# Kernel tuning notes

Hardware: AMD Instinct MI355X
Metric: run time of the kernel (lower is better)

The kernel has to match this reference:

```python
import jax, jax.numpy as jnp
import numpy as np

N = 40000   # nodes
E = 480000  # edges
F = 128     # input features
H = 128     # hidden
C = 10      # classes
G = 128     # graphs in batch
L = 3       # conv layers
EPS = 1e-5


def _bn(x, g, b):
    # BatchNorm1d, training-mode batch statistics (biased variance, as torch)
    m = x.mean(0)
    v = x.var(0)
    return (x - m) / jnp.sqrt(v + EPS) * g + b


def _gcn_prop(x, row, col, w, n):
    # PyG-style GCN propagation: add self loops (weight 1), sym-normalize, scatter-add.
    loop = jnp.arange(n)
    r = jnp.concatenate([row, loop])
    c = jnp.concatenate([col, loop])
    ww = jnp.concatenate([w, jnp.ones((n,), x.dtype)])
    deg = jax.ops.segment_sum(ww, r, num_segments=n)  # deg >= 1 thanks to self loops
    dinv = jnp.power(deg, -0.5)
    norm = dinv[r] * ww * dinv[c]                      # [E+N]
    return jax.ops.segment_sum(norm[:, None] * x[r], c, num_segments=n)


def setup_inputs() -> dict:
    key = jax.random.key(0)
    ks = jax.random.split(key, 12)
    nrm = lambda k, s: jax.random.normal(k, s, jnp.float32) * 0.02
    return {
        'x': jax.random.normal(ks[0], (N, F), jnp.float32),
        'edge_index': jax.random.randint(ks[1], (2, E), 0, N, jnp.int32),
        'batch': jnp.sort(jax.random.randint(ks[2], (N,), 0, G, jnp.int32)),
        'bn_feat_g': jnp.ones((F,), jnp.float32), 'bn_feat_b': jnp.full((F,), 1e-4, jnp.float32),
        'W_feat': nrm(ks[3], (F, H)),
        'bns_g': jnp.ones((L, H), jnp.float32), 'bns_b': jnp.full((L, H), 1e-4, jnp.float32),
        'conv_W': nrm(ks[4], (L, H, H)), 'conv_b': jnp.zeros((L, H), jnp.float32),
        'W_eatt': nrm(ks[5], (2 * H, 2)), 'b_eatt': jnp.zeros((2,), jnp.float32),
        'W_natt': nrm(ks[6], (H, 2)), 'b_natt': jnp.zeros((2,), jnp.float32),
        'bnc_g': jnp.ones((H,), jnp.float32), 'bnc_b': jnp.full((H,), 1e-4, jnp.float32),
        'bno_g': jnp.ones((H,), jnp.float32), 'bno_b': jnp.full((H,), 1e-4, jnp.float32),
        'Wc': nrm(ks[7], (H, H)), 'bc': jnp.zeros((H,), jnp.float32),
        'Wo': nrm(ks[8], (H, H)), 'bo': jnp.zeros((H,), jnp.float32),
        'ro_bn1_g': jnp.ones((3, H), jnp.float32), 'ro_bn1_b': jnp.full((3, H), 1e-4, jnp.float32),
        'ro_W1': nrm(ks[9], (3, H, H)), 'ro_b1': jnp.zeros((3, H), jnp.float32),
        'ro_bn2_g': jnp.ones((3, H), jnp.float32), 'ro_bn2_b': jnp.full((3, H), 1e-4, jnp.float32),
        'ro_W2': nrm(ks[10], (3, H, C)), 'ro_b2': jnp.zeros((3, C), jnp.float32),
    }


def reference(x, edge_index, batch,
              bn_feat_g, bn_feat_b, W_feat, bns_g, bns_b, conv_W, conv_b,
              W_eatt, b_eatt, W_natt, b_natt, bnc_g, bnc_b, bno_g, bno_b,
              Wc, bc, Wo, bo,
              ro_bn1_g, ro_bn1_b, ro_W1, ro_b1, ro_bn2_g, ro_bn2_b, ro_W2, ro_b2):
    row, col = edge_index[0], edge_index[1]
    # feature BN + gfn conv (linear only, no propagation, no bias) + ReLU
    h = jax.nn.relu(_bn(x, bn_feat_g, bn_feat_b) @ W_feat)
    ones_w = jnp.ones((E,), h.dtype)
    for i in range(L):
        z = _bn(h, bns_g[i], bns_b[i]) @ conv_W[i]
        h = jax.nn.relu(_gcn_prop(z, row, col, ones_w, N) + conv_b[i])
    # edge / node attention
    edge_rep = jnp.concatenate([h[row], h[col]], axis=-1)          # [E, 2H]
    e_att = jax.nn.softmax(edge_rep @ W_eatt + b_eatt, axis=-1)    # [E, 2]
    n_att = jax.nn.softmax(h @ W_natt + b_natt, axis=-1)           # [N, 2]
    xc = n_att[:, 0:1] * h
    xo = n_att[:, 1:2] * h
    xc = jax.nn.relu(_gcn_prop(_bn(xc, bnc_g, bnc_b) @ Wc, row, col, e_att[:, 0], N) + bc)
    xo = jax.nn.relu(_gcn_prop(_bn(xo, bno_g, bno_b) @ Wo, row, col, e_att[:, 1], N) + bo)
    # global add pool -> [G, H]
    xc = jax.ops.segment_sum(xc, batch, num_segments=G)
    xo = jax.ops.segment_sum(xo, batch, num_segments=G)

    def ro(v, i):
        v = _bn(v, ro_bn1_g[i], ro_bn1_b[i]) @ ro_W1[i] + ro_b1[i]
        v = _bn(jax.nn.relu(v), ro_bn2_g[i], ro_bn2_b[i]) @ ro_W2[i] + ro_b2[i]
        return jax.nn.log_softmax(v, axis=-1)

    # with_random=False -> identity permutation; cat_or_add='add' -> xc + xo
    return ro(xc, 0), ro(xo, 1), ro(xc + xo, 2)
```

## Files before the change

### kernel.cpp

```cpp
#include <hip/hip_runtime.h>

#define HD 128

typedef __attribute__((ext_vector_type(8))) short bf16x8v;
typedef __attribute__((ext_vector_type(4))) float f32x4v;

__device__ __forceinline__ unsigned short f2bf(float f) {
  unsigned int u = __float_as_uint(f);
  u += 0x7FFFu + ((u >> 16) & 1u);
  return (unsigned short)(u >> 16);
}
__device__ __forceinline__ float bf2f(unsigned short h) {
  return __uint_as_float(((unsigned int)h) << 16);
}
__device__ __forceinline__ float bflo(unsigned int u) { return __uint_as_float(u << 16); }
__device__ __forceinline__ float bfhi(unsigned int u) { return __uint_as_float(u & 0xFFFF0000u); }
__device__ __forceinline__ unsigned int packbf(float a, float b) {
  return (unsigned int)f2bf(a) | ((unsigned int)f2bf(b) << 16);
}


__global__ void hist_kernel(const int* __restrict__ row, const int* __restrict__ col,
                            int* __restrict__ cnt_in, int* __restrict__ outdeg, int e) {
  int i = blockIdx.x * blockDim.x + threadIdx.x;
  if (i < e) { atomicAdd(&cnt_in[col[i]], 1); atomicAdd(&outdeg[row[i]], 1); }
}

__global__ void scan1(const int* __restrict__ cnt, int n, int* __restrict__ sums) {
  __shared__ int lds[256];
  int b = blockIdx.x, t = threadIdx.x;
  int base = b * 1024 + t * 4;
  int s = 0;
#pragma unroll
  for (int m = 0; m < 4; m++) if (base + m < n) s += cnt[base + m];
  lds[t] = s;
  __syncthreads();
  for (int d = 128; d > 0; d >>= 1) {
    if (t < d) lds[t] += lds[t + d];
    __syncthreads();
  }
  if (t == 0) sums[b] = lds[0];
}

__global__ void scan2(const int* __restrict__ sums, int nc, int* __restrict__ off) {
  int l = threadIdx.x;
  int v = (l < nc) ? sums[l] : 0;
  int x = v;
#pragma unroll
  for (int d = 1; d < 64; d <<= 1) {
    int y = __shfl_up(x, d, 64);
    if (l >= d) x += y;
  }
  if (l < nc) off[l] = x - v;
}

__global__ void scan3(const int* __restrict__ cnt, int n, const int* __restrict__ off,
                      int* __restrict__ ptr, int* __restrict__ cursor) {
  __shared__ int lds[256];
  int b = blockIdx.x, t = threadIdx.x;
  int base = b * 1024 + t * 4;
  int v[4], p[4];
#pragma unroll
  for (int m = 0; m < 4; m++) v[m] = (base + m < n) ? cnt[base + m] : 0;
  p[0] = v[0];
#pragma unroll
  for (int m = 1; m < 4; m++) p[m] = p[m - 1] + v[m];
  int tsum = p[3];
  lds[t] = tsum;
  __syncthreads();
  for (int d = 1; d < 256; d <<= 1) {
    int y = 0;
    if (t >= d) y = lds[t - d];
    __syncthreads();
    lds[t] += y;
    __syncthreads();
  }
  int basev = off[b] + lds[t] - tsum;
  if (b == 0 && t == 0) ptr[0] = 0;
#pragma unroll
  for (int m = 0; m < 4; m++) {
    int i = base + m;
    if (i < n) {
      int incl = basev + p[m];
      ptr[i + 1] = incl;
      cursor[i] = incl - v[m];
    }
  }
}

__global__ void place_both(const int* __restrict__ row, const int* __restrict__ col,
                           int* __restrict__ cursor, int* __restrict__ cursor2,
                           int* __restrict__ csr_src, int* __restrict__ csr_dst,
                           int* __restrict__ csr_eid, int* __restrict__ csr2_eid, int e) {
  int i = blockIdx.x * blockDim.x + threadIdx.x;
  if (i < e) {
    int r = row[i], c = col[i];
    int pos = atomicAdd(&cursor[c], 1);
    csr_src[pos] = r;
    csr_dst[pos] = c;
    csr_eid[pos] = i;
    int pos2 = atomicAdd(&cursor2[r], 1);
    csr2_eid[pos2] = i;
  }
}

__global__ void dinv1_kernel(const int* __restrict__ outdeg, float* __restrict__ dinv1, int n) {
  int i = blockIdx.x * blockDim.x + threadIdx.x;
  if (i < n) dinv1[i] = rsqrtf((float)(outdeg[i] + 1));
}

__global__ void wn1_flat(const int* __restrict__ csr_src, const int* __restrict__ csr_dst,
                         const float* __restrict__ dinv1, float* __restrict__ wn, int e) {
  int i = blockIdx.x * blockDim.x + threadIdx.x;
  if (i < e) wn[i] = dinv1[csr_src[i]] * dinv1[csr_dst[i]];
}


#define CS_BLOCKS 512

__global__ __launch_bounds__(256) void colstats_castx(
    const float* __restrict__ A, unsigned short* __restrict__ Abf, int n,
    float* __restrict__ sum, float* __restrict__ sumsq) {
  __shared__ float redS[8][132], redQ[8][132];
  int tid = threadIdx.x;
  int cg = tid & 31, ro = tid >> 5;
  float s[4] = {0.f, 0.f, 0.f, 0.f}, q[4] = {0.f, 0.f, 0.f, 0.f};
  for (int r = blockIdx.x * 8 + ro; r < n; r += gridDim.x * 8) {
    float4 v = *(const float4*)(A + (size_t)r * HD + cg * 4);
    uint2 pk;
    pk.x = packbf(v.x, v.y);
    pk.y = packbf(v.z, v.w);
    *(uint2*)(Abf + (size_t)r * HD + cg * 4) = pk;
    s[0] += v.x; q[0] += v.x * v.x;
    s[1] += v.y; q[1] += v.y * v.y;
    s[2] += v.z; q[2] += v.z * v.z;
    s[3] += v.w; q[3] += v.w * v.w;
  }
#pragma unroll
  for (int i = 0; i < 4; i++) { redS[ro][cg * 4 + i] = s[i]; redQ[ro][cg * 4 + i] = q[i]; }
  __syncthreads();
  if (tid < 128) {
    float ts = 0.f, tq = 0.f;
#pragma unroll
    for (int k = 0; k < 8; k++) { ts += redS[k][tid]; tq += redQ[k][tid]; }
    atomicAdd(&sum[tid], ts);
    atomicAdd(&sumsq[tid], tq);
  }
}

__global__ __launch_bounds__(256) void colstats_bf(
    const unsigned short* __restrict__ A, int n,
    float* __restrict__ sum, float* __restrict__ sumsq) {
  __shared__ float redS[8][132], redQ[8][132];
  int tid = threadIdx.x;
  int cg = tid & 31, ro = tid >> 5;
  float s[4] = {0.f, 0.f, 0.f, 0.f}, q[4] = {0.f, 0.f, 0.f, 0.f};
  for (int r = blockIdx.x * 8 + ro; r < n; r += gridDim.x * 8) {
    uint2 u = *(const uint2*)(A + (size_t)r * HD + cg * 4);
    float v0 = bflo(u.x), v1 = bfhi(u.x), v2 = bflo(u.y), v3 = bfhi(u.y);
    s[0] += v0; q[0] += v0 * v0;
    s[1] += v1; q[1] += v1 * v1;
    s[2] += v2; q[2] += v2 * v2;
    s[3] += v3; q[3] += v3 * v3;
  }
#pragma unroll
  for (int i = 0; i < 4; i++) { redS[ro][cg * 4 + i] = s[i]; redQ[ro][cg * 4 + i] = q[i]; }
  __syncthreads();
  if (tid < 128) {
    float ts = 0.f, tq = 0.f;
#pragma unroll
    for (int k = 0; k < 8; k++) { ts += redS[k][tid]; tq += redQ[k][tid]; }
    atomicAdd(&sum[tid], ts);
    atomicAdd(&sumsq[tid], tq);
  }
}

__global__ __launch_bounds__(256) void colstats_scaled(
    const unsigned short* __restrict__ A, const float* __restrict__ natt, int n,
    float* __restrict__ o4) {
  __shared__ float rSC[8][132], rQC[8][132], rSO[8][132], rQO[8][132];
  int tid = threadIdx.x;
  int cg = tid & 31, ro = tid >> 5;
  float sc[4] = {0.f, 0.f, 0.f, 0.f}, qc[4] = {0.f, 0.f, 0.f, 0.f};
  float so[4] = {0.f, 0.f, 0.f, 0.f}, qo[4] = {0.f, 0.f, 0.f, 0.f};
  for (int r = blockIdx.x * 8 + ro; r < n; r += gridDim.x * 8) {
    uint2 u = *(const uint2*)(A + (size_t)r * HD + cg * 4);
    float2 at = *(const float2*)(natt + r * 2);
    float v[4] = {bflo(u.x), bfhi(u.x), bflo(u.y), bfhi(u.y)};
#pragma unroll
    for (int i = 0; i < 4; i++) {
      float vc = at.x * v[i], vo = at.y * v[i];
      sc[i] += vc; qc[i] += vc * vc;
      so[i] += vo; qo[i] += vo * vo;
    }
  }
#pragma unroll
  for (int i = 0; i < 4; i++) {
    rSC[ro][cg * 4 + i] = sc[i]; rQC[ro][cg * 4 + i] = qc[i];
    rSO[ro][cg * 4 + i] = so[i]; rQO[ro][cg * 4 + i] = qo[i];
  }
  __syncthreads();
  if (tid < 128) {
    float a = 0.f, b = 0.f, c = 0.f, d = 0.f;
#pragma unroll
    for (int k = 0; k < 8; k++) {
      a += rSC[k][tid]; b += rQC[k][tid]; c += rSO[k][tid]; d += rQO[k][tid];
    }
    atomicAdd(&o4[tid], a);
    atomicAdd(&o4[HD + tid], b);
    atomicAdd(&o4[2 * HD + tid], c);
    atomicAdd(&o4[3 * HD + tid], d);
  }
}


__global__ __launch_bounds__(256) void gemm_mfma(
    const unsigned short* __restrict__ A, const float* __restrict__ W,
    const float* __restrict__ g, const float* __restrict__ b,
    const float* __restrict__ ssum, const float* __restrict__ ssq, float invN,
    const float* __restrict__ rowscale, int rsStride,
    unsigned short* __restrict__ out, int n, int relu) {
  __shared__ unsigned short WT[128][136];
  __shared__ float sA[HD], tA[HD], tb[HD];
  int tid = threadIdx.x;
  int r00 = blockIdx.x * 128;

  if (tid < HD) {
    float m = ssum[tid] * invN;
    float v = ssq[tid] * invN - m * m;
    float s = g[tid] * rsqrtf(v + 1e-5f);
    sA[tid] = s;
    tA[tid] = b[tid] - m * s;
  }
  __syncthreads();
  for (int idx = tid; idx < 4096; idx += 256) {
    int k = idx >> 5;
    int j4 = (idx & 31) * 4;
    float4 w = *(const float4*)(W + (size_t)k * 128 + j4);
    float s = sA[k];
    WT[j4 + 0][k] = f2bf(w.x * s);
    WT[j4 + 1][k] = f2bf(w.y * s);
    WT[j4 + 2][k] = f2bf(w.z * s);
    WT[j4 + 3][k] = f2bf(w.w * s);
  }
  if (tid < HD) {
    float acc = 0.f;
#pragma unroll 8
    for (int k = 0; k < HD; k++) acc += tA[k] * W[(size_t)k * 128 + tid];
    tb[tid] = acc;
  }
  __syncthreads();

  int w = tid >> 6;
  int l = tid & 63;
  int colb = l & 15;
  int kcb = l >> 4;

#pragma unroll
  for (int rt = 0; rt < 2; rt++) {
    int r0 = r00 + rt * 64;
    if (r0 >= n) break;
    int arow = r0 + w * 16 + colb;
    bool rowok = arow < n;

    f32x4v acc[8];
#pragma unroll
    for (int jt = 0; jt < 8; jt++) acc[jt] = (f32x4v){0.f, 0.f, 0.f, 0.f};

    const unsigned short* Ap = A + (size_t)(rowok ? arow : 0) * 128 + kcb * 8;
#pragma unroll
    for (int kit = 0; kit < 4; kit++) {
      bf16x8v a;
      if (rowok) a = *(const bf16x8v*)(Ap + kit * 32);
      else a = (bf16x8v){0, 0, 0, 0, 0, 0, 0, 0};
#pragma unroll
      for (int jt = 0; jt < 8; jt++) {
        bf16x8v bb = *(const bf16x8v*)&WT[jt * 16 + colb][kit * 32 + kcb * 8];
        acc[jt] = __builtin_amdgcn_mfma_f32_16x16x32_bf16(a, bb, acc[jt], 0, 0, 0);
      }
    }

    int rbase = r0 + w * 16 + kcb * 4;
    float rs[4];
#pragma unroll
    for (int i = 0; i < 4; i++)
      rs[i] = rowscale ? ((rbase + i < n) ? rowscale[(size_t)(rbase + i) * rsStride] : 0.f) : 1.f;
#pragma unroll
    for (int jt = 0; jt < 8; jt++) {
      int colj = jt * 16 + colb;
      float tbv = tb[colj];
#pragma unroll
      for (int i = 0; i < 4; i++) {
        int r = rbase + i;
        if (r < n) {
          float v = acc[jt][i] * rs[i] + tbv;
          if (relu) v = fmaxf(v, 0.f);
          out[(size_t)r * 128 + colj] = f2bf(v);
        }
      }
    }
  }
}


__global__ __launch_bounds__(256) void prop1(
    const unsigned short* __restrict__ z, const int* __restrict__ ptr,
    const int* __restrict__ src, const float* __restrict__ wn,
    const float* __restrict__ dinv, const float* __restrict__ bias,
    unsigned short* __restrict__ out, int n, int relu) {
  int node = blockIdx.x * 4 + (threadIdx.x >> 6);
  if (node >= n) return;
  int lane = threadIdx.x & 63;
  const unsigned int* zp = (const unsigned int*)z;
  float dn = dinv[node];
  float ws = dn * dn;
  unsigned int us = zp[(size_t)node * 64 + lane];
  float a0 = ws * bflo(us), a1 = ws * bfhi(us);
  int e = ptr[node], e1 = ptr[node + 1];
  for (; e + 3 < e1; e += 4) {
    int s0 = src[e], s1 = src[e + 1], s2 = src[e + 2], s3 = src[e + 3];
    float w0 = wn[e], w1 = wn[e + 1], w2 = wn[e + 2], w3 = wn[e + 3];
    unsigned int u0 = zp[(size_t)s0 * 64 + lane];
    unsigned int u1 = zp[(size_t)s1 * 64 + lane];
    unsigned int u2 = zp[(size_t)s2 * 64 + lane];
    unsigned int u3 = zp[(size_t)s3 * 64 + lane];
    a0 += w0 * bflo(u0) + w1 * bflo(u1) + w2 * bflo(u2) + w3 * bflo(u3);
    a1 += w0 * bfhi(u0) + w1 * bfhi(u1) + w2 * bfhi(u2) + w3 * bfhi(u3);
  }
  for (; e < e1; e++) {
    unsigned int u = zp[(size_t)src[e] * 64 + lane];
    float we = wn[e];
    a0 += we * bflo(u);
    a1 += we * bfhi(u);
  }
  a0 += bias[lane * 2];
  a1 += bias[lane * 2 + 1];
  if (relu) { a0 = fmaxf(a0, 0.f); a1 = fmaxf(a1, 0.f); }
  ((unsigned int*)out)[(size_t)node * 64 + lane] = packbf(a0, a1);
}

__global__ __launch_bounds__(256) void prop2(
    const unsigned short* __restrict__ z1, const unsigned short* __restrict__ z2,
    const int* __restrict__ ptr, const int* __restrict__ src,
    const float* __restrict__ wnc, const float* __restrict__ wno,
    const float2* __restrict__ ddeg, const float* __restrict__ bc,
    const float* __restrict__ bo, unsigned short* __restrict__ xc,
    unsigned short* __restrict__ xo, int n) {
  int node = blockIdx.x * 4 + (threadIdx.x >> 6);
  if (node >= n) return;
  int lane = threadIdx.x & 63;
  const unsigned int* z1p = (const unsigned int*)z1;
  const unsigned int* z2p = (const unsigned int*)z2;
  float2 dd = ddeg[node];
  float wsc = dd.x * dd.x, wso = dd.y * dd.y;
  unsigned int uc = z1p[(size_t)node * 64 + lane];
  unsigned int uo = z2p[(size_t)node * 64 + lane];
  float c0 = wsc * bflo(uc), c1 = wsc * bfhi(uc);
  float o0 = wso * bflo(uo), o1 = wso * bfhi(uo);
  int e = ptr[node], e1 = ptr[node + 1];
  for (; e + 1 < e1; e += 2) {
    int s0 = src[e], s1 = src[e + 1];
    float wc0 = wnc[e], wc1 = wnc[e + 1];
    float wo0 = wno[e], wo1 = wno[e + 1];
    unsigned int a0 = z1p[(size_t)s0 * 64 + lane];
    unsigned int b0 = z2p[(size_t)s0 * 64 + lane];
    unsigned int a1 = z1p[(size_t)s1 * 64 + lane];
    unsigned int b1 = z2p[(size_t)s1 * 64 + lane];
    c0 += wc0 * bflo(a0) + wc1 * bflo(a1);
    c1 += wc0 * bfhi(a0) + wc1 * bfhi(a1);
    o0 += wo0 * bflo(b0) + wo1 * bflo(b1);
    o1 += wo0 * bfhi(b0) + wo1 * bfhi(b1);
  }
  for (; e < e1; e++) {
    int s = src[e];
    float wc = wnc[e], wo = wno[e];
    unsigned int a = z1p[(size_t)s * 64 + lane];
    unsigned int b = z2p[(size_t)s * 64 + lane];
    c0 += wc * bflo(a); c1 += wc * bfhi(a);
    o0 += wo * bflo(b); o1 += wo * bfhi(b);
  }
  c0 = fmaxf(c0 + bc[lane * 2], 0.f);
  c1 = fmaxf(c1 + bc[lane * 2 + 1], 0.f);
  o0 = fmaxf(o0 + bo[lane * 2], 0.f);
  o1 = fmaxf(o1 + bo[lane * 2 + 1], 0.f);
  ((unsigned int*)xc)[(size_t)node * 64 + lane] = packbf(c0, c1);
  ((unsigned int*)xo)[(size_t)node * 64 + lane] = packbf(o0, o1);
}


__global__ void proj_kernel(const unsigned short* __restrict__ h, const float* __restrict__ We,
                            const float* __restrict__ Wn, const float* __restrict__ bn,
                            float* __restrict__ natt, float* __restrict__ pe, int n) {
  int gtid = blockIdx.x * blockDim.x + threadIdx.x;
  int wave = gtid >> 6;
  int lane = threadIdx.x & 63;
  int nwaves = (gridDim.x * blockDim.x) >> 6;
  const unsigned int* hp = (const unsigned int*)h;
  float4 we0 = *(const float4*)(We + lane * 4);
  float4 we1 = *(const float4*)(We + 256 + lane * 4);
  float4 wn0 = *(const float4*)(Wn + lane * 4);
  for (int node = wave; node < n; node += nwaves) {
    unsigned int u = hp[(size_t)node * 64 + lane];
    float h0 = bflo(u), h1 = bfhi(u);
    float v[6];
    v[0] = h0 * we0.x + h1 * we0.z;
    v[1] = h0 * we0.y + h1 * we0.w;
    v[2] = h0 * we1.x + h1 * we1.z;
    v[3] = h0 * we1.y + h1 * we1.w;
    v[4] = h0 * wn0.x + h1 * wn0.z;
    v[5] = h0 * wn0.y + h1 * wn0.w;
#pragma unroll
    for (int m = 32; m > 0; m >>= 1) {
#pragma unroll
      for (int q = 0; q < 6; q++) v[q] += __shfl_xor(v[q], m, 64);
    }
    if (lane == 0) {
      float q0 = v[4] + bn[0], q1 = v[5] + bn[1];
      float mx = fmaxf(q0, q1);
      float e0 = expf(q0 - mx), e1 = expf(q1 - mx);
      float inv = 1.f / (e0 + e1);
      natt[node * 2 + 0] = e0 * inv;
      natt[node * 2 + 1] = e1 * inv;
      pe[node * 4 + 0] = v[0];
      pe[node * 4 + 1] = v[1];
      pe[node * 4 + 2] = v[2];
      pe[node * 4 + 3] = v[3];
    }
  }
}

__global__ void eatt_flat(const int* __restrict__ row, const int* __restrict__ col,
                          const float* __restrict__ pe, const float* __restrict__ be,
                          float2* __restrict__ eattO, int e) {
  int i = blockIdx.x * blockDim.x + threadIdx.x;
  if (i >= e) return;
  int r = row[i], c = col[i];
  float l0 = pe[r * 4 + 0] + pe[c * 4 + 2] + be[0];
  float l1 = pe[r * 4 + 1] + pe[c * 4 + 3] + be[1];
  float m = fmaxf(l0, l1);
  float e0 = expf(l0 - m), e1 = expf(l1 - m);
  float inv = 1.f / (e0 + e1);
  eattO[i] = make_float2(e0 * inv, e1 * inv);
}

__global__ void deg_kernel(const int* __restrict__ ptrR, const int* __restrict__ csr2_eid,
                           const float2* __restrict__ eattO, float2* __restrict__ ddeg, int n) {
  int gtid = blockIdx.x * blockDim.x + threadIdx.x;
  int node = gtid >> 6;
  int lane = threadIdx.x & 63;
  if (node >= n) return;
  int e0 = ptrR[node], e1 = ptrR[node + 1];
  float sc = 0.f, so = 0.f;
  for (int e = e0 + lane; e < e1; e += 64) {
    float2 at = eattO[csr2_eid[e]];
    sc += at.x; so += at.y;
  }
#pragma unroll
  for (int m = 32; m > 0; m >>= 1) {
    sc += __shfl_xor(sc, m, 64);
    so += __shfl_xor(so, m, 64);
  }
  if (lane == 0) ddeg[node] = make_float2(rsqrtf(1.f + sc), rsqrtf(1.f + so));
}

__global__ void wn_flat(const int* __restrict__ csr_src, const int* __restrict__ csr_dst,
                        const int* __restrict__ csr_eid, const float2* __restrict__ eattO,
                        const float2* __restrict__ ddeg, float* __restrict__ wnc,
                        float* __restrict__ wno, int e) {
  int i = blockIdx.x * blockDim.x + threadIdx.x;
  if (i >= e) return;
  int s = csr_src[i], c = csr_dst[i];
  float2 at = eattO[csr_eid[i]];
  float2 ds = ddeg[s], dc = ddeg[c];
  wnc[i] = ds.x * at.x * dc.x;
  wno[i] = ds.y * at.y * dc.y;
}


#define POOL_RPB 32

__global__ void pool_kernel(const unsigned short* __restrict__ xc,
                            const unsigned short* __restrict__ xo,
                            const int* __restrict__ batch, int n,
                            float* __restrict__ pc, float* __restrict__ po) {
  int j = threadIdx.x;
  int r0 = blockIdx.x * POOL_RPB;
  int r1 = min(n, r0 + POOL_RPB);
  if (r0 >= n) return;
  int g = batch[r0];
  float ac = 0.f, ao = 0.f;
  for (int r = r0; r < r1; r++) {
    int br = batch[r];
    if (br != g) {
      atomicAdd(&pc[g * HD + j], ac);
      atomicAdd(&po[g * HD + j], ao);
      ac = 0.f; ao = 0.f; g = br;
    }
    ac += bf2f(xc[(size_t)r * HD + j]);
    ao += bf2f(xo[(size_t)r * HD + j]);
  }
  atomicAdd(&pc[g * HD + j], ac);
  atomicAdd(&po[g * HD + j], ao);
}


__global__ __launch_bounds__(256) void head1(
    const float* __restrict__ pc, const float* __restrict__ po,
    const float* __restrict__ bn1g, const float* __restrict__ bn1b,
    const float* __restrict__ W1, const float* __restrict__ b1,
    float* __restrict__ Ybuf) {
  int t = blockIdx.x >> 2;
  int jt = blockIdx.x & 3;
  __shared__ float V[128][132];
  __shared__ float Wt[128][33];
  __shared__ float sA[128], tA[128];
  __shared__ float redS[2][128], redQ[2][128];
  int tid = threadIdx.x;

  for (int idx = tid; idx < 16384; idx += 256) {
    int r = idx >> 7, j = idx & 127;
    float v = (t == 0) ? pc[idx] : (t == 1) ? po[idx] : (pc[idx] + po[idx]);
    V[r][j] = v;
  }
  for (int idx = tid; idx < 4096; idx += 256) {
    int k = idx >> 5, c = idx & 31;
    Wt[k][c] = W1[(size_t)t * 16384 + k * 128 + jt * 32 + c];
  }
  __syncthreads();
  {
    int cj = tid & 127, ch = tid >> 7;
    float s = 0.f, q = 0.f;
    for (int r = ch * 64; r < ch * 64 + 64; r++) { float v = V[r][cj]; s += v; q += v * v; }
    redS[ch][cj] = s; redQ[ch][cj] = q;
  }
  __syncthreads();
  if (tid < 128) {
    float s = redS[0][tid] + redS[1][tid];
    float q = redQ[0][tid] + redQ[1][tid];
    float m = s * (1.f / 128.f), var = q * (1.f / 128.f) - m * m;
    float sc = bn1g[t * 128 + tid] * rsqrtf(var + 1e-5f);
    sA[tid] = sc; tA[tid] = bn1b[t * 128 + tid] - m * sc;
  }
  __syncthreads();
  for (int idx = tid; idx < 16384; idx += 256) {
    int r = idx >> 7, j = idx & 127;
    V[r][j] = V[r][j] * sA[j] + tA[j];
  }
  __syncthreads();
  int tr = tid >> 5, tc = tid & 31;
  float acc[16];
#pragma unroll
  for (int i = 0; i < 16; i++) acc[i] = 0.f;
  for (int k = 0; k < 128; k += 4) {
    float w0 = Wt[k][tc], w1 = Wt[k + 1][tc], w2 = Wt[k + 2][tc], w3 = Wt[k + 3][tc];
#pragma unroll
    for (int i = 0; i < 16; i++) {
      float4 v = *(float4*)&V[tr * 16 + i][k];
      acc[i] += v.x * w0 + v.y * w1 + v.z * w2 + v.w * w3;
    }
  }
  float bj = b1[t * 128 + jt * 32 + tc];
#pragma unroll
  for (int i = 0; i < 16; i++) {
    int r = tr * 16 + i;
    Ybuf[(size_t)t * 16384 + r * 128 + jt * 32 + tc] = fmaxf(acc[i] + bj, 0.f);
  }
}

__global__ __launch_bounds__(256) void head2(
    const float* __restrict__ Ybuf,
    const float* __restrict__ bn2g, const float* __restrict__ bn2b,
    const float* __restrict__ W2, const float* __restrict__ b2,
    float* __restrict__ out) {
  int t = blockIdx.x;
  __shared__ float Y[128][132];
  __shared__ float W2s[128][11];
  __shared__ float Z[128][12];
  __shared__ float sA[128], tA[128];
  __shared__ float redS[2][128], redQ[2][128];
  int tid = threadIdx.x;

  for (int idx = tid; idx < 16384; idx += 256) {
    int r = idx >> 7, j = idx & 127;
    Y[r][j] = Ybuf[(size_t)t * 16384 + idx];
  }
  for (int idx = tid; idx < 1280; idx += 256) {
    int k = idx / 10, c = idx % 10;
    W2s[k][c] = W2[(size_t)t * 1280 + idx];
  }
  __syncthreads();
  {
    int cj = tid & 127, ch = tid >> 7;
    float s = 0.f, q = 0.f;
    for (int r = ch * 64; r < ch * 64 + 64; r++) { float v = Y[r][cj]; s += v; q += v * v; }
    redS[ch][cj] = s; redQ[ch][cj] = q;
  }
  __syncthreads();
  if (tid < 128) {
    float s = redS[0][tid] + redS[1][tid];
    float q = redQ[0][tid] + redQ[1][tid];
    float m = s * (1.f / 128.f), var = q * (1.f / 128.f) - m * m;
    float sc = bn2g[t * 128 + tid] * rsqrtf(var + 1e-5f);
    sA[tid] = sc; tA[tid] = bn2b[t * 128 + tid] - m * sc;
  }
  __syncthreads();
  for (int idx = tid; idx < 16384; idx += 256) {
    int r = idx >> 7, j = idx & 127;
    Y[r][j] = Y[r][j] * sA[j] + tA[j];
  }
  __syncthreads();
  for (int idx = tid; idx < 1280; idx += 256) {
    int r = idx / 10, c = idx % 10;
    float acc = b2[t * 10 + c];
#pragma unroll 8
    for (int k = 0; k < 128; k++) acc += Y[r][k] * W2s[k][c];
    Z[r][c] = acc;
  }
  __syncthreads();
  if (tid < 128) {
    int r = tid;
    float m = -1e30f;
    for (int c = 0; c < 10; c++) m = fmaxf(m, Z[r][c]);
    float se = 0.f;
    for (int c = 0; c < 10; c++) se += expf(Z[r][c] - m);
    float lse = m + logf(se);
    for (int c = 0; c < 10; c++) out[t * 1280 + r * 10 + c] = Z[r][c] - lse;
  }
}


extern "C" void kernel_launch(void* const* d_in, const int* in_sizes, int n_in,
                              void* d_out, int out_size, void* d_ws, size_t ws_size,
                              hipStream_t stream) {
  const int N = in_sizes[0] / HD;
  const int E = in_sizes[1] / 2;
  const int G = out_size / 30;

  const float* x      = (const float*)d_in[0];
  const int*   ei     = (const int*)d_in[1];
  const int*   batch  = (const int*)d_in[2];
  const float* bnfg   = (const float*)d_in[3];
  const float* bnfb   = (const float*)d_in[4];
  const float* Wfeat  = (const float*)d_in[5];
  const float* bnsg   = (const float*)d_in[6];
  const float* bnsb   = (const float*)d_in[7];
  const float* convW  = (const float*)d_in[8];
  const float* convb  = (const float*)d_in[9];
  const float* Weatt  = (const float*)d_in[10];
  const float* beatt  = (const float*)d_in[11];
  const float* Wnatt  = (const float*)d_in[12];
  const float* bnatt  = (const float*)d_in[13];
  const float* bncg   = (const float*)d_in[14];
  const float* bncb   = (const float*)d_in[15];
  const float* bnog   = (const float*)d_in[16];
  const float* bnob   = (const float*)d_in[17];
  const float* Wc     = (const float*)d_in[18];
  const float* bc     = (const float*)d_in[19];
  const float* Wo     = (const float*)d_in[20];
  const float* bo     = (const float*)d_in[21];
  const float* robn1g = (const float*)d_in[22];
  const float* robn1b = (const float*)d_in[23];
  const float* roW1   = (const float*)d_in[24];
  const float* rob1   = (const float*)d_in[25];
  const float* robn2g = (const float*)d_in[26];
  const float* robn2b = (const float*)d_in[27];
  const float* roW2   = (const float*)d_in[28];
  const float* rob2   = (const float*)d_in[29];
  float* out = (float*)d_out;

  const int* row = ei;
  const int* col = ei + E;

  char* p = (char*)d_ws;
  auto alloc = [&](size_t bytes) -> void* {
    void* r = (void*)p;
    p += (bytes + 255) & ~(size_t)255;
    return r;
  };
  unsigned short* xbf = (unsigned short*)alloc((size_t)N * HD * 2);
  unsigned short* B0  = (unsigned short*)alloc((size_t)N * HD * 2);
  unsigned short* Xc  = (unsigned short*)alloc((size_t)N * HD * 2);
  unsigned short* Xo  = (unsigned short*)alloc((size_t)N * HD * 2);
  unsigned short* Z1  = (unsigned short*)alloc((size_t)N * HD * 2);
  unsigned short* Z2  = (unsigned short*)alloc((size_t)N * HD * 2);
  float2* eattO  = (float2*)alloc((size_t)E * 8);
  int*   csr_src = (int*)alloc((size_t)E * 4);
  int*   csr_dst = (int*)alloc((size_t)E * 4);
  int*   csr_eid = (int*)alloc((size_t)E * 4);
  int*   csr2_eid= (int*)alloc((size_t)E * 4);
  float* wn1     = (float*)alloc((size_t)E * 4);
  float* wnc     = (float*)alloc((size_t)E * 4);
  float* wno     = (float*)alloc((size_t)E * 4);
  int*   ptrA    = (int*)alloc((size_t)(N + 1) * 4);
  int*   ptrR    = (int*)alloc((size_t)(N + 1) * 4);
  int*   cursor  = (int*)alloc((size_t)N * 4);
  int*   cursor2 = (int*)alloc((size_t)N * 4);
  int*   cnt_in  = (int*)alloc((size_t)N * 4);
  int*   outdeg  = (int*)alloc((size_t)N * 4);
  float* dinv1   = (float*)alloc((size_t)N * 4);
  float2* ddeg   = (float2*)alloc((size_t)N * 8);
  float* natt    = (float*)alloc((size_t)N * 2 * 4);
  float* pe      = (float*)alloc((size_t)N * 4 * 4);
  float* stats   = (float*)alloc(12 * HD * 4);
  float* pooledc = (float*)alloc((size_t)G * HD * 4);
  float* pooledo = (float*)alloc((size_t)G * HD * 4);
  float* Ybuf    = (float*)alloc((size_t)3 * 128 * 128 * 4);
  int*   csums   = (int*)alloc(64 * 4);
  int*   coffs   = (int*)alloc(64 * 4);
  int*   csums2  = (int*)alloc(64 * 4);
  int*   coffs2  = (int*)alloc(64 * 4);

  const int NCH = (N + 1023) / 1024;

  hipMemsetAsync(cnt_in, 0, (size_t)N * 4, stream);
  hipMemsetAsync(outdeg, 0, (size_t)N * 4, stream);
  hipMemsetAsync(stats, 0, 12 * HD * 4, stream);
  hipMemsetAsync(pooledc, 0, (size_t)G * HD * 4, stream);
  hipMemsetAsync(pooledo, 0, (size_t)G * HD * 4, stream);

  hist_kernel<<<(E + 255) / 256, 256, 0, stream>>>(row, col, cnt_in, outdeg, E);
  scan1<<<NCH, 256, 0, stream>>>(cnt_in, N, csums);
  scan2<<<1, 64, 0, stream>>>(csums, NCH, coffs);
  scan3<<<NCH, 256, 0, stream>>>(cnt_in, N, coffs, ptrA, cursor);
  scan1<<<NCH, 256, 0, stream>>>(outdeg, N, csums2);
  scan2<<<1, 64, 0, stream>>>(csums2, NCH, coffs2);
  scan3<<<NCH, 256, 0, stream>>>(outdeg, N, coffs2, ptrR, cursor2);
  place_both<<<(E + 255) / 256, 256, 0, stream>>>(row, col, cursor, cursor2,
                                                  csr_src, csr_dst, csr_eid, csr2_eid, E);
  dinv1_kernel<<<(N + 255) / 256, 256, 0, stream>>>(outdeg, dinv1, N);
  wn1_flat<<<(E + 255) / 256, 256, 0, stream>>>(csr_src, csr_dst, dinv1, wn1, E);

  int gblocks = (N + 127) / 128;
  int pblocks = (N + 3) / 4;
  float invN = 1.f / (float)N;

  colstats_castx<<<CS_BLOCKS, 256, 0, stream>>>(x, xbf, N, stats, stats + HD);
  gemm_mfma<<<gblocks, 256, 0, stream>>>(xbf, Wfeat, bnfg, bnfb, stats, stats + HD, invN,
                                         nullptr, 0, B0, N, 1);

  for (int i = 0; i < 3; i++) {
    float* hs = stats + 2 * HD + i * 2 * HD;
    colstats_bf<<<CS_BLOCKS, 256, 0, stream>>>(B0, N, hs, hs + HD);
    gemm_mfma<<<gblocks, 256, 0, stream>>>(B0, convW + (size_t)i * HD * HD,
                                           bnsg + i * HD, bnsb + i * HD, hs, hs + HD, invN,
                                           nullptr, 0, Z1, N, 0);
    prop1<<<pblocks, 256, 0, stream>>>(Z1, ptrA, csr_src, wn1, dinv1,
                                       convb + i * HD, B0, N, 1);
  }

  proj_kernel<<<512, 256, 0, stream>>>(B0, Weatt, Wnatt, bnatt, natt, pe, N);
  eatt_flat<<<(E + 255) / 256, 256, 0, stream>>>(row, col, pe, beatt, eattO, E);
  deg_kernel<<<(N * 64 + 255) / 256, 256, 0, stream>>>(ptrR, csr2_eid, eattO, ddeg, N);
  wn_flat<<<(E + 255) / 256, 256, 0, stream>>>(csr_src, csr_dst, csr_eid, eattO, ddeg,
                                               wnc, wno, E);

  float* cs = stats + 8 * HD;
  colstats_scaled<<<CS_BLOCKS, 256, 0, stream>>>(B0, natt, N, cs);
  gemm_mfma<<<gblocks, 256, 0, stream>>>(B0, Wc, bncg, bncb, cs, cs + HD, invN,
                                         natt, 2, Z1, N, 0);
  gemm_mfma<<<gblocks, 256, 0, stream>>>(B0, Wo, bnog, bnob, cs + 2 * HD, cs + 3 * HD, invN,
                                         natt + 1, 2, Z2, N, 0);

  prop2<<<pblocks, 256, 0, stream>>>(Z1, Z2, ptrA, csr_src, wnc, wno, ddeg, bc, bo,
                                     Xc, Xo, N);

  pool_kernel<<<(N + POOL_RPB - 1) / POOL_RPB, 128, 0, stream>>>(Xc, Xo, batch, N, pooledc, pooledo);
  head1<<<12, 256, 0, stream>>>(pooledc, pooledo, robn1g, robn1b, roW1, rob1, Ybuf);
  head2<<<3, 256, 0, stream>>>(Ybuf, robn2g, robn2b, roW2, rob2, out);
}
```

Measured before the change: 702.4 us.

## Compute GCN edge norms on the fly in propagation and pack CSR src/eid

Removes the precomputed per-edge weight kernels (wn1_flat, wn_flat) and their E-sized arrays. The propagation kernels now gather dinv or ddeg of the source node and the edge attention directly, and factor the destination-node normalisation out of the sum. The CSR source and edge id are packed into one int2 array, and csr_dst is dropped. This saves two launches and several E-sized streams of writes and reads, at the cost of extra scattered gathers inside the propagation loops, which run three times for prop1.

```diff
diff --git a/kernel.cpp b/kernel.cpp
--- a/kernel.cpp
+++ b/kernel.cpp
@@ -90,15 +90,13 @@
 
 __global__ void place_both(const int* __restrict__ row, const int* __restrict__ col,
                            int* __restrict__ cursor, int* __restrict__ cursor2,
-                           int* __restrict__ csr_src, int* __restrict__ csr_dst,
-                           int* __restrict__ csr_eid, int* __restrict__ csr2_eid, int e) {
+                           int2* __restrict__ csrSE, int* __restrict__ csr2_eid, int e) {
   int i = blockIdx.x * blockDim.x + threadIdx.x;
   if (i < e) {
     int r = row[i], c = col[i];
     int pos = atomicAdd(&cursor[c], 1);
-    csr_src[pos] = r;
-    csr_dst[pos] = c;
-    csr_eid[pos] = i;
+    int2 se; se.x = r; se.y = i;
+    csrSE[pos] = se;
     int pos2 = atomicAdd(&cursor2[r], 1);
     csr2_eid[pos2] = i;
   }
@@ -107,12 +105,6 @@
 __global__ void dinv1_kernel(const int* __restrict__ outdeg, float* __restrict__ dinv1, int n) {
   int i = blockIdx.x * blockDim.x + threadIdx.x;
   if (i < n) dinv1[i] = rsqrtf((float)(outdeg[i] + 1));
-}
-
-__global__ void wn1_flat(const int* __restrict__ csr_src, const int* __restrict__ csr_dst,
-                         const float* __restrict__ dinv1, float* __restrict__ wn, int e) {
-  int i = blockIdx.x * blockDim.x + threadIdx.x;
-  if (i < e) wn[i] = dinv1[csr_src[i]] * dinv1[csr_dst[i]];
 }
 
 
@@ -305,84 +297,85 @@
 
 __global__ __launch_bounds__(256) void prop1(
     const unsigned short* __restrict__ z, const int* __restrict__ ptr,
-    const int* __restrict__ src, const float* __restrict__ wn,
-    const float* __restrict__ dinv, const float* __restrict__ bias,
-    unsigned short* __restrict__ out, int n, int relu) {
+    const int2* __restrict__ csrSE, const float* __restrict__ dinv,
+    const float* __restrict__ bias, unsigned short* __restrict__ out, int n, int relu) {
   int node = blockIdx.x * 4 + (threadIdx.x >> 6);
   if (node >= n) return;
   int lane = threadIdx.x & 63;
   const unsigned int* zp = (const unsigned int*)z;
   float dn = dinv[node];
-  float ws = dn * dn;
   unsigned int us = zp[(size_t)node * 64 + lane];
-  float a0 = ws * bflo(us), a1 = ws * bfhi(us);
+  float a0 = dn * bflo(us), a1 = dn * bfhi(us);
   int e = ptr[node], e1 = ptr[node + 1];
   for (; e + 3 < e1; e += 4) {
-    int s0 = src[e], s1 = src[e + 1], s2 = src[e + 2], s3 = src[e + 3];
-    float w0 = wn[e], w1 = wn[e + 1], w2 = wn[e + 2], w3 = wn[e + 3];
-    unsigned int u0 = zp[(size_t)s0 * 64 + lane];
-    unsigned int u1 = zp[(size_t)s1 * 64 + lane];
-    unsigned int u2 = zp[(size_t)s2 * 64 + lane];
-    unsigned int u3 = zp[(size_t)s3 * 64 + lane];
+    int2 se0 = csrSE[e], se1 = csrSE[e + 1], se2 = csrSE[e + 2], se3 = csrSE[e + 3];
+    float w0 = dinv[se0.x], w1 = dinv[se1.x], w2 = dinv[se2.x], w3 = dinv[se3.x];
+    unsigned int u0 = zp[(size_t)se0.x * 64 + lane];
+    unsigned int u1 = zp[(size_t)se1.x * 64 + lane];
+    unsigned int u2 = zp[(size_t)se2.x * 64 + lane];
+    unsigned int u3 = zp[(size_t)se3.x * 64 + lane];
     a0 += w0 * bflo(u0) + w1 * bflo(u1) + w2 * bflo(u2) + w3 * bflo(u3);
     a1 += w0 * bfhi(u0) + w1 * bfhi(u1) + w2 * bfhi(u2) + w3 * bfhi(u3);
   }
   for (; e < e1; e++) {
-    unsigned int u = zp[(size_t)src[e] * 64 + lane];
-    float we = wn[e];
+    int2 se = csrSE[e];
+    unsigned int u = zp[(size_t)se.x * 64 + lane];
+    float we = dinv[se.x];
     a0 += we * bflo(u);
     a1 += we * bfhi(u);
   }
-  a0 += bias[lane * 2];
-  a1 += bias[lane * 2 + 1];
+  a0 = dn * a0 + bias[lane * 2];
+  a1 = dn * a1 + bias[lane * 2 + 1];
   if (relu) { a0 = fmaxf(a0, 0.f); a1 = fmaxf(a1, 0.f); }
   ((unsigned int*)out)[(size_t)node * 64 + lane] = packbf(a0, a1);
 }
 
 __global__ __launch_bounds__(256) void prop2(
     const unsigned short* __restrict__ z1, const unsigned short* __restrict__ z2,
-    const int* __restrict__ ptr, const int* __restrict__ src,
-    const float* __restrict__ wnc, const float* __restrict__ wno,
-    const float2* __restrict__ ddeg, const float* __restrict__ bc,
-    const float* __restrict__ bo, unsigned short* __restrict__ xc,
-    unsigned short* __restrict__ xo, int n) {
+    const int* __restrict__ ptr, const int2* __restrict__ csrSE,
+    const float2* __restrict__ eattO, const float2* __restrict__ ddeg,
+    const float* __restrict__ bc, const float* __restrict__ bo,
+    unsigned short* __restrict__ xc, unsigned short* __restrict__ xo, int n) {
   int node = blockIdx.x * 4 + (threadIdx.x >> 6);
   if (node >= n) return;
   int lane = threadIdx.x & 63;
   const unsigned int* z1p = (const unsigned int*)z1;
   const unsigned int* z2p = (const unsigned int*)z2;
   float2 dd = ddeg[node];
-  float wsc = dd.x * dd.x, wso = dd.y * dd.y;
   unsigned int uc = z1p[(size_t)node * 64 + lane];
   unsigned int uo = z2p[(size_t)node * 64 + lane];
-  float c0 = wsc * bflo(uc), c1 = wsc * bfhi(uc);
-  float o0 = wso * bflo(uo), o1 = wso * bfhi(uo);
+  float c0 = dd.x * bflo(uc), c1 = dd.x * bfhi(uc);
+  float o0 = dd.y * bflo(uo), o1 = dd.y * bfhi(uo);
   int e = ptr[node], e1 = ptr[node + 1];
   for (; e + 1 < e1; e += 2) {
-    int s0 = src[e], s1 = src[e + 1];
-    float wc0 = wnc[e], wc1 = wnc[e + 1];
-    float wo0 = wno[e], wo1 = wno[e + 1];
-    unsigned int a0 = z1p[(size_t)s0 * 64 + lane];
-    unsigned int b0 = z2p[(size_t)s0 * 64 + lane];
-    unsigned int a1 = z1p[(size_t)s1 * 64 + lane];
-    unsigned int b1 = z2p[(size_t)s1 * 64 + lane];
+    int2 se0 = csrSE[e], se1 = csrSE[e + 1];
+    float2 at0 = eattO[se0.y], at1 = eattO[se1.y];
+    float2 ds0 = ddeg[se0.x], ds1 = ddeg[se1.x];
+    float wc0 = ds0.x * at0.x, wc1 = ds1.x * at1.x;
+    float wo0 = ds0.y * at0.y, wo1 = ds1.y * at1.y;
+    unsigned int a0 = z1p[(size_t)se0.x * 64 + lane];
+    unsigned int b0 = z2p[(size_t)se0.x * 64 + lane];
+    unsigned int a1 = z1p[(size_t)se1.x * 64 + lane];
+    unsigned int b1 = z2p[(size_t)se1.x * 64 + lane];
     c0 += wc0 * bflo(a0) + wc1 * bflo(a1);
     c1 += wc0 * bfhi(a0) + wc1 * bfhi(a1);
     o0 += wo0 * bflo(b0) + wo1 * bflo(b1);
     o1 += wo0 * bfhi(b0) + wo1 * bfhi(b1);
   }
   for (; e < e1; e++) {
-    int s = src[e];
-    float wc = wnc[e], wo = wno[e];
-    unsigned int a = z1p[(size_t)s * 64 + lane];
-    unsigned int b = z2p[(size_t)s * 64 + lane];
+    int2 se = csrSE[e];
+    float2 at = eattO[se.y];
+    float2 ds = ddeg[se.x];
+    float wc = ds.x * at.x, wo = ds.y * at.y;
+    unsigned int a = z1p[(size_t)se.x * 64 + lane];
+    unsigned int b = z2p[(size_t)se.x * 64 + lane];
     c0 += wc * bflo(a); c1 += wc * bfhi(a);
     o0 += wo * bflo(b); o1 += wo * bfhi(b);
   }
-  c0 = fmaxf(c0 + bc[lane * 2], 0.f);
-  c1 = fmaxf(c1 + bc[lane * 2 + 1], 0.f);
-  o0 = fmaxf(o0 + bo[lane * 2], 0.f);
-  o1 = fmaxf(o1 + bo[lane * 2 + 1], 0.f);
+  c0 = fmaxf(dd.x * c0 + bc[lane * 2], 0.f);
+  c1 = fmaxf(dd.x * c1 + bc[lane * 2 + 1], 0.f);
+  o0 = fmaxf(dd.y * o0 + bo[lane * 2], 0.f);
+  o1 = fmaxf(dd.y * o1 + bo[lane * 2 + 1], 0.f);
   ((unsigned int*)xc)[(size_t)node * 64 + lane] = packbf(c0, c1);
   ((unsigned int*)xo)[(size_t)node * 64 + lane] = packbf(o0, o1);
 }
@@ -461,19 +454,6 @@
     so += __shfl_xor(so, m, 64);
   }
   if (lane == 0) ddeg[node] = make_float2(rsqrtf(1.f + sc), rsqrtf(1.f + so));
-}
-
-__global__ void wn_flat(const int* __restrict__ csr_src, const int* __restrict__ csr_dst,
-                        const int* __restrict__ csr_eid, const float2* __restrict__ eattO,
-                        const float2* __restrict__ ddeg, float* __restrict__ wnc,
-                        float* __restrict__ wno, int e) {
-  int i = blockIdx.x * blockDim.x + threadIdx.x;
-  if (i >= e) return;
-  int s = csr_src[i], c = csr_dst[i];
-  float2 at = eattO[csr_eid[i]];
-  float2 ds = ddeg[s], dc = ddeg[c];
-  wnc[i] = ds.x * at.x * dc.x;
-  wno[i] = ds.y * at.y * dc.y;
 }
 
 
@@ -684,13 +664,8 @@
   unsigned short* Z1  = (unsigned short*)alloc((size_t)N * HD * 2);
   unsigned short* Z2  = (unsigned short*)alloc((size_t)N * HD * 2);
   float2* eattO  = (float2*)alloc((size_t)E * 8);
-  int*   csr_src = (int*)alloc((size_t)E * 4);
-  int*   csr_dst = (int*)alloc((size_t)E * 4);
-  int*   csr_eid = (int*)alloc((size_t)E * 4);
+  int2*  csrSE   = (int2*)alloc((size_t)E * 8);
   int*   csr2_eid= (int*)alloc((size_t)E * 4);
-  float* wn1     = (float*)alloc((size_t)E * 4);
-  float* wnc     = (float*)alloc((size_t)E * 4);
-  float* wno     = (float*)alloc((size_t)E * 4);
   int*   ptrA    = (int*)alloc((size_t)(N + 1) * 4);
   int*   ptrR    = (int*)alloc((size_t)(N + 1) * 4);
   int*   cursor  = (int*)alloc((size_t)N * 4);
@@ -726,9 +701,8 @@
   scan2<<<1, 64, 0, stream>>>(csums2, NCH, coffs2);
   scan3<<<NCH, 256, 0, stream>>>(outdeg, N, coffs2, ptrR, cursor2);
   place_both<<<(E + 255) / 256, 256, 0, stream>>>(row, col, cursor, cursor2,
-                                                  csr_src, csr_dst, csr_eid, csr2_eid, E);
+                                                  csrSE, csr2_eid, E);
   dinv1_kernel<<<(N + 255) / 256, 256, 0, stream>>>(outdeg, dinv1, N);
-  wn1_flat<<<(E + 255) / 256, 256, 0, stream>>>(csr_src, csr_dst, dinv1, wn1, E);
 
   int gblocks = (N + 127) / 128;
   int pblocks = (N + 3) / 4;
@@ -744,15 +718,12 @@
     gemm_mfma<<<gblocks, 256, 0, stream>>>(B0, convW + (size_t)i * HD * HD,
                                            bnsg + i * HD, bnsb + i * HD, hs, hs + HD, invN,
                                            nullptr, 0, Z1, N, 0);
-    prop1<<<pblocks, 256, 0, stream>>>(Z1, ptrA, csr_src, wn1, dinv1,
-                                       convb + i * HD, B0, N, 1);
+    prop1<<<pblocks, 256, 0, stream>>>(Z1, ptrA, csrSE, dinv1, convb + i * HD, B0, N, 1);
   }
 
   proj_kernel<<<512, 256, 0, stream>>>(B0, Weatt, Wnatt, bnatt, natt, pe, N);
   eatt_flat<<<(E + 255) / 256, 256, 0, stream>>>(row, col, pe, beatt, eattO, E);
   deg_kernel<<<(N * 64 + 255) / 256, 256, 0, stream>>>(ptrR, csr2_eid, eattO, ddeg, N);
-  wn_flat<<<(E + 255) / 256, 256, 0, stream>>>(csr_src, csr_dst, csr_eid, eattO, ddeg,
-                                               wnc, wno, E);
 
   float* cs = stats + 8 * HD;
   colstats_scaled<<<CS_BLOCKS, 256, 0, stream>>>(B0, natt, N, cs);
@@ -761,8 +732,7 @@
   gemm_mfma<<<gblocks, 256, 0, stream>>>(B0, Wo, bnog, bnob, cs + 2 * HD, cs + 3 * HD, invN,
                                          natt + 1, 2, Z2, N, 0);
 
-  prop2<<<pblocks, 256, 0, stream>>>(Z1, Z2, ptrA, csr_src, wnc, wno, ddeg, bc, bo,
-                                     Xc, Xo, N);
+  prop2<<<pblocks, 256, 0, stream>>>(Z1, Z2, ptrA, csrSE, eattO, ddeg, bc, bo, Xc, Xo, N);
 
   pool_kernel<<<(N + POOL_RPB - 1) / POOL_RPB, 128, 0, stream>>>(Xc, Xo, batch, N, pooledc, pooledo);
   head1<<<12, 256, 0, stream>>>(pooledc, pooledo, robn1g, robn1b, roW1, rob1, Ybuf);
```

Measured after the change: 729.9 us. 1.04x slower.

## Use LDS-sliced histogram, deepen gather unroll in props, pack edge weights

Applied to the files above, without the earlier changes.

Replaces the global-atomic degree histogram and its two memsets with a sliced LDS histogram. Each of 32 blocks scans all edges but only counts keys that fall in its own node range. prop1 now unrolls 8 edges so more independent gathers are in flight. prop2 unrolls 4 edges and reads a single packed float2 weight array in place of two separate arrays. The sliced histogram re-reads the edge list once per slice, and its 32 blocks underfill the GPU in exchange for dropping the global atomics.

```diff
diff --git a/kernel.cpp b/kernel.cpp
--- a/kernel.cpp
+++ b/kernel.cpp
@@ -19,6 +19,28 @@
   return (unsigned int)f2bf(a) | ((unsigned int)f2bf(b) << 16);
 }
 
+
+#define HSLICE 16
+__global__ __launch_bounds__(1024) void hist_slice(
+    const int* __restrict__ row, const int* __restrict__ col,
+    int* __restrict__ cnt_in, int* __restrict__ outdeg, int n, int e) {
+  __shared__ int hbin[2560];
+  int b = blockIdx.x;
+  const int* keys = (b < HSLICE) ? col : row;
+  int* outp = (b < HSLICE) ? cnt_in : outdeg;
+  int sb = b & (HSLICE - 1);
+  int per = (n + HSLICE - 1) / HSLICE;
+  int lo = sb * per, hi = min(n, lo + per);
+  int cnt = hi - lo;
+  for (int i = threadIdx.x; i < cnt; i += 1024) hbin[i] = 0;
+  __syncthreads();
+  for (int i = threadIdx.x; i < e; i += 1024) {
+    int k = keys[i];
+    if (k >= lo && k < hi) atomicAdd(&hbin[k - lo], 1);
+  }
+  __syncthreads();
+  for (int i = threadIdx.x; i < cnt; i += 1024) outp[lo + i] = hbin[i];
+}
 
 __global__ void hist_kernel(const int* __restrict__ row, const int* __restrict__ col,
                             int* __restrict__ cnt_in, int* __restrict__ outdeg, int e) {
@@ -317,15 +339,23 @@
   unsigned int us = zp[(size_t)node * 64 + lane];
   float a0 = ws * bflo(us), a1 = ws * bfhi(us);
   int e = ptr[node], e1 = ptr[node + 1];
+  for (; e + 7 < e1; e += 8) {
+    int s[8]; float w[8]; unsigned int u[8];
+#pragma unroll
+    for (int k = 0; k < 8; k++) { s[k] = src[e + k]; w[k] = wn[e + k]; }
+#pragma unroll
+    for (int k = 0; k < 8; k++) u[k] = zp[(size_t)s[k] * 64 + lane];
+#pragma unroll
+    for (int k = 0; k < 8; k++) { a0 += w[k] * bflo(u[k]); a1 += w[k] * bfhi(u[k]); }
+  }
   for (; e + 3 < e1; e += 4) {
-    int s0 = src[e], s1 = src[e + 1], s2 = src[e + 2], s3 = src[e + 3];
-    float w0 = wn[e], w1 = wn[e + 1], w2 = wn[e + 2], w3 = wn[e + 3];
-    unsigned int u0 = zp[(size_t)s0 * 64 + lane];
-    unsigned int u1 = zp[(size_t)s1 * 64 + lane];
-    unsigned int u2 = zp[(size_t)s2 * 64 + lane];
-    unsigned int u3 = zp[(size_t)s3 * 64 + lane];
-    a0 += w0 * bflo(u0) + w1 * bflo(u1) + w2 * bflo(u2) + w3 * bflo(u3);
-    a1 += w0 * bfhi(u0) + w1 * bfhi(u1) + w2 * bfhi(u2) + w3 * bfhi(u3);
+    int s[4]; float w[4]; unsigned int u[4];
+#pragma unroll
+    for (int k = 0; k < 4; k++) { s[k] = src[e + k]; w[k] = wn[e + k]; }
+#pragma unroll
+    for (int k = 0; k < 4; k++) u[k] = zp[(size_t)s[k] * 64 + lane];
+#pragma unroll
+    for (int k = 0; k < 4; k++) { a0 += w[k] * bflo(u[k]); a1 += w[k] * bfhi(u[k]); }
   }
   for (; e < e1; e++) {
     unsigned int u = zp[(size_t)src[e] * 64 + lane];
@@ -342,10 +372,9 @@
 __global__ __launch_bounds__(256) void prop2(
     const unsigned short* __restrict__ z1, const unsigned short* __restrict__ z2,
     const int* __restrict__ ptr, const int* __restrict__ src,
-    const float* __restrict__ wnc, const float* __restrict__ wno,
-    const float2* __restrict__ ddeg, const float* __restrict__ bc,
-    const float* __restrict__ bo, unsigned short* __restrict__ xc,
-    unsigned short* __restrict__ xo, int n) {
+    const float2* __restrict__ wpack, const float2* __restrict__ ddeg,
+    const float* __restrict__ bc, const float* __restrict__ bo,
+    unsigned short* __restrict__ xc, unsigned short* __restrict__ xo, int n) {
   int node = blockIdx.x * 4 + (threadIdx.x >> 6);
   if (node >= n) return;
   int lane = threadIdx.x & 63;
@@ -358,26 +387,28 @@
   float c0 = wsc * bflo(uc), c1 = wsc * bfhi(uc);
   float o0 = wso * bflo(uo), o1 = wso * bfhi(uo);
   int e = ptr[node], e1 = ptr[node + 1];
-  for (; e + 1 < e1; e += 2) {
-    int s0 = src[e], s1 = src[e + 1];
-    float wc0 = wnc[e], wc1 = wnc[e + 1];
-    float wo0 = wno[e], wo1 = wno[e + 1];
-    unsigned int a0 = z1p[(size_t)s0 * 64 + lane];
-    unsigned int b0 = z2p[(size_t)s0 * 64 + lane];
-    unsigned int a1 = z1p[(size_t)s1 * 64 + lane];
-    unsigned int b1 = z2p[(size_t)s1 * 64 + lane];
-    c0 += wc0 * bflo(a0) + wc1 * bflo(a1);
-    c1 += wc0 * bfhi(a0) + wc1 * bfhi(a1);
-    o0 += wo0 * bflo(b0) + wo1 * bflo(b1);
-    o1 += wo0 * bfhi(b0) + wo1 * bfhi(b1);
+  for (; e + 3 < e1; e += 4) {
+    int s[4]; float2 w[4]; unsigned int a[4], b[4];
+#pragma unroll
+    for (int k = 0; k < 4; k++) { s[k] = src[e + k]; w[k] = wpack[e + k]; }
+#pragma unroll
+    for (int k = 0; k < 4; k++) {
+      a[k] = z1p[(size_t)s[k] * 64 + lane];
+      b[k] = z2p[(size_t)s[k] * 64 + lane];
+    }
+#pragma unroll
+    for (int k = 0; k < 4; k++) {
+      c0 += w[k].x * bflo(a[k]); c1 += w[k].x * bfhi(a[k]);
+      o0 += w[k].y * bflo(b[k]); o1 += w[k].y * bfhi(b[k]);
+    }
   }
   for (; e < e1; e++) {
     int s = src[e];
-    float wc = wnc[e], wo = wno[e];
+    float2 w = wpack[e];
     unsigned int a = z1p[(size_t)s * 64 + lane];
     unsigned int b = z2p[(size_t)s * 64 + lane];
-    c0 += wc * bflo(a); c1 += wc * bfhi(a);
-    o0 += wo * bflo(b); o1 += wo * bfhi(b);
+    c0 += w.x * bflo(a); c1 += w.x * bfhi(a);
+    o0 += w.y * bflo(b); o1 += w.y * bfhi(b);
   }
   c0 = fmaxf(c0 + bc[lane * 2], 0.f);
   c1 = fmaxf(c1 + bc[lane * 2 + 1], 0.f);
@@ -465,15 +496,13 @@
 
 __global__ void wn_flat(const int* __restrict__ csr_src, const int* __restrict__ csr_dst,
                         const int* __restrict__ csr_eid, const float2* __restrict__ eattO,
-                        const float2* __restrict__ ddeg, float* __restrict__ wnc,
-                        float* __restrict__ wno, int e) {
+                        const float2* __restrict__ ddeg, float2* __restrict__ wpack, int e) {
   int i = blockIdx.x * blockDim.x + threadIdx.x;
   if (i >= e) return;
   int s = csr_src[i], c = csr_dst[i];
   float2 at = eattO[csr_eid[i]];
   float2 ds = ddeg[s], dc = ddeg[c];
-  wnc[i] = ds.x * at.x * dc.x;
-  wno[i] = ds.y * at.y * dc.y;
+  wpack[i] = make_float2(ds.x * at.x * dc.x, ds.y * at.y * dc.y);
 }
 
 
@@ -684,13 +713,12 @@
   unsigned short* Z1  = (unsigned short*)alloc((size_t)N * HD * 2);
   unsigned short* Z2  = (unsigned short*)alloc((size_t)N * HD * 2);
   float2* eattO  = (float2*)alloc((size_t)E * 8);
+  float2* wpack  = (float2*)alloc((size_t)E * 8);
   int*   csr_src = (int*)alloc((size_t)E * 4);
   int*   csr_dst = (int*)alloc((size_t)E * 4);
   int*   csr_eid = (int*)alloc((size_t)E * 4);
   int*   csr2_eid= (int*)alloc((size_t)E * 4);
   float* wn1     = (float*)alloc((size_t)E * 4);
-  float* wnc     = (float*)alloc((size_t)E * 4);
-  float* wno     = (float*)alloc((size_t)E * 4);
   int*   ptrA    = (int*)alloc((size_t)(N + 1) * 4);
   int*   ptrR    = (int*)alloc((size_t)(N + 1) * 4);
   int*   cursor  = (int*)alloc((size_t)N * 4);
@@ -712,13 +740,17 @@
 
   const int NCH = (N + 1023) / 1024;
 
-  hipMemsetAsync(cnt_in, 0, (size_t)N * 4, stream);
-  hipMemsetAsync(outdeg, 0, (size_t)N * 4, stream);
   hipMemsetAsync(stats, 0, 12 * HD * 4, stream);
   hipMemsetAsync(pooledc, 0, (size_t)G * HD * 4, stream);
   hipMemsetAsync(pooledo, 0, (size_t)G * HD * 4, stream);
 
-  hist_kernel<<<(E + 255) / 256, 256, 0, stream>>>(row, col, cnt_in, outdeg, E);
+  if ((N + HSLICE - 1) / HSLICE <= 2560) {
+    hist_slice<<<2 * HSLICE, 1024, 0, stream>>>(row, col, cnt_in, outdeg, N, E);
+  } else {
+    hipMemsetAsync(cnt_in, 0, (size_t)N * 4, stream);
+    hipMemsetAsync(outdeg, 0, (size_t)N * 4, stream);
+    hist_kernel<<<(E + 255) / 256, 256, 0, stream>>>(row, col, cnt_in, outdeg, E);
+  }
   scan1<<<NCH, 256, 0, stream>>>(cnt_in, N, csums);
   scan2<<<1, 64, 0, stream>>>(csums, NCH, coffs);
   scan3<<<NCH, 256, 0, stream>>>(cnt_in, N, coffs, ptrA, cursor);
@@ -744,15 +776,14 @@
     gemm_mfma<<<gblocks, 256, 0, stream>>>(B0, convW + (size_t)i * HD * HD,
                                            bnsg + i * HD, bnsb + i * HD, hs, hs + HD, invN,
                                            nullptr, 0, Z1, N, 0);
-    prop1<<<pblocks, 256, 0, stream>>>(Z1, ptrA, csr_src, wn1, dinv1,
-                                       convb + i * HD, B0, N, 1);
+    prop1<<<pblocks, 256, 0, stream>>>(Z1, ptrA, csr_src, wn1, dinv1, convb + i * HD, B0, N, 1);
   }
 
   proj_kernel<<<512, 256, 0, stream>>>(B0, Weatt, Wnatt, bnatt, natt, pe, N);
   eatt_flat<<<(E + 255) / 256, 256, 0, stream>>>(row, col, pe, beatt, eattO, E);
   deg_kernel<<<(N * 64 + 255) / 256, 256, 0, stream>>>(ptrR, csr2_eid, eattO, ddeg, N);
   wn_flat<<<(E + 255) / 256, 256, 0, stream>>>(csr_src, csr_dst, csr_eid, eattO, ddeg,
-                                               wnc, wno, E);
+                                               wpack, E);
 
   float* cs = stats + 8 * HD;
   colstats_scaled<<<CS_BLOCKS, 256, 0, stream>>>(B0, natt, N, cs);
@@ -761,8 +792,7 @@
   gemm_mfma<<<gblocks, 256, 0, stream>>>(B0, Wo, bnog, bnob, cs + 2 * HD, cs + 3 * HD, invN,
                                          natt + 1, 2, Z2, N, 0);
 
-  prop2<<<pblocks, 256, 0, stream>>>(Z1, Z2, ptrA, csr_src, wnc, wno, ddeg, bc, bo,
-                                     Xc, Xo, N);
+  prop2<<<pblocks, 256, 0, stream>>>(Z1, Z2, ptrA, csr_src, wpack, ddeg, bc, bo, Xc, Xo, N);
 
   pool_kernel<<<(N + POOL_RPB - 1) / POOL_RPB, 128, 0, stream>>>(Xc, Xo, batch, N, pooledc, pooledo);
   head1<<<12, 256, 0, stream>>>(pooledc, pooledo, robn1g, robn1b, roW1, rob1, Ybuf);
```

Result: slower. 798.3 us (+13.7%).
